# Performance work log

Measured on AMD Instinct MI355X. Metric: run time of the kernel, lower is better.

## Reference

```python
import jax, jax.numpy as jnp
import numpy as np
from jax import lax

B, S, H, T = 64, 512, 1024, 48


def setup_inputs() -> dict:
    key = jax.random.key(0)
    ks = jax.random.split(key, 8)
    x = jax.random.normal(ks[0], (B, S, H), dtype=jnp.float32)
    # left-aligned variable-length attention mask (lengths in [S//2, S])
    lengths = jax.random.randint(ks[1], (B,), S // 2, S + 1)
    attention_mask = (jnp.arange(S)[None, :] < lengths[:, None]).astype(jnp.int32)
    labels = jax.random.randint(ks[2], (B, S), 0, T).astype(jnp.int64)
    # decoder Linear(H, T)
    W = jax.random.normal(ks[3], (H, T), dtype=jnp.float32) / np.sqrt(H)
    b = jnp.zeros((T,), dtype=jnp.float32)
    # CRF parameters (allennlp-style: transitions + start/end transitions)
    transitions = jax.random.normal(ks[4], (T, T), dtype=jnp.float32) * 0.1
    start_trans = jax.random.normal(ks[5], (T,), dtype=jnp.float32) * 0.1
    end_trans = jax.random.normal(ks[6], (T,), dtype=jnp.float32) * 0.1
    return {"x": x, "attention_mask": attention_mask, "labels": labels,
            "W": W, "b": b, "transitions": transitions,
            "start_trans": start_trans, "end_trans": end_trans}


def _log_partition(logits, mask, trans, start, end):
    # logits [B,S,T], mask [B,S] int. Returns logZ [B].
    alpha0 = start[None, :] + logits[:, 0]                     # [B,T]
    emits = jnp.moveaxis(logits[:, 1:], 1, 0)                  # [S-1,B,T]
    ms = mask[:, 1:].T                                         # [S-1,B]

    def step(alpha, inp):
        emit, m = inp
        inner = alpha[:, :, None] + trans[None, :, :] + emit[:, None, :]  # [B,T,T]
        new = jax.nn.logsumexp(inner, axis=1)
        alpha = jnp.where(m[:, None] > 0, new, alpha)
        return alpha, None

    alpha, _ = lax.scan(step, alpha0, (emits, ms))
    return jax.nn.logsumexp(alpha + end[None, :], axis=1)      # [B]


def _gold_score(logits, labels, mask, trans, start, end):
    maskf = mask.astype(logits.dtype)
    emit = jnp.take_along_axis(logits, labels[..., None], axis=2)[..., 0]  # [B,S]
    emit_score = jnp.sum(emit * maskf, axis=1)
    tr = trans[labels[:, :-1], labels[:, 1:]]                   # [B,S-1]
    trans_score = jnp.sum(tr * maskf[:, 1:], axis=1)
    last_idx = jnp.sum(mask, axis=1) - 1                        # [B]
    last_tags = jnp.take_along_axis(labels, last_idx[:, None], axis=1)[:, 0]
    return start[labels[:, 0]] + emit_score + trans_score + end[last_tags]


def _viterbi(logits, mask, trans, start, end):
    Bn, Sn, Tn = logits.shape
    v0 = start[None, :] + logits[:, 0]
    emits = jnp.moveaxis(logits[:, 1:], 1, 0)                  # [S-1,B,T]
    ms = mask[:, 1:].T
    ident = jnp.broadcast_to(jnp.arange(Tn, dtype=jnp.int32)[None, :], (Bn, Tn))

    def step(v, inp):
        emit, m = inp
        scores = v[:, :, None] + trans[None, :, :]              # [B,T_prev,T_cur]
        bp = jnp.argmax(scores, axis=1).astype(jnp.int32)       # [B,T]
        best = jnp.max(scores, axis=1) + emit
        v_new = jnp.where(m[:, None] > 0, best, v)
        bp = jnp.where(m[:, None] > 0, bp, ident)               # identity at padded steps
        return v_new, bp

    v, bps = lax.scan(step, v0, (emits, ms))                    # bps [S-1,B,T]
    last = jnp.argmax(v + end[None, :], axis=1).astype(jnp.int32)  # [B]

    def back(tag, bp):
        prev = jnp.take_along_axis(bp, tag[:, None], axis=1)[:, 0]
        return prev, tag

    first_tag, rest = lax.scan(back, last, bps, reverse=True)   # rest [S-1,B]
    tags = jnp.concatenate([first_tag[:, None], rest.T], axis=1)  # [B,S]
    return (tags * mask).astype(jnp.int64)                      # pad with zeros


def reference(x, attention_mask, labels, W, b, transitions, start_trans, end_trans):
    features = jnp.einsum('bsh,ht->bst', x, W) + b              # decoder Linear
    pred_labels = _viterbi(features, attention_mask, transitions, start_trans, end_trans)
    logZ = _log_partition(features, attention_mask, transitions, start_trans, end_trans)
    gold = _gold_score(features, labels, attention_mask, transitions, start_trans, end_trans)
    loss = -jnp.sum(gold - logZ)                                # -log-likelihood, summed over batch
    return features, pred_labels, loss
```

## Files before the change

### kernel.cpp

```cpp
#include <hip/hip_runtime.h>
#include <hip/hip_bf16.h>
#include <math.h>

#define Bn 64
#define Sn 512
#define Hn 1024
#define Tn 48

#define LOG2E 1.4426950408889634f
#define LN2f  0.6931471805599453f

#define PRED_OFF (Bn*Sn*Tn)
#define LOSS_OFF (PRED_OFF + Bn*Sn)

#define RL(x,i) __int_as_float(__builtin_amdgcn_readlane(__float_as_int(x),(i)))

#if __has_builtin(__builtin_amdgcn_exp2f)
#define EXP2(x) __builtin_amdgcn_exp2f(x)
#else
#define EXP2(x) exp2f(x)
#endif
#if __has_builtin(__builtin_amdgcn_logf)
#define LOG2(x) __builtin_amdgcn_logf(x)
#else
#define LOG2(x) log2f(x)
#endif

__device__ __forceinline__ unsigned umin2(unsigned a, unsigned b) { return a < b ? a : b; }

#define DOT4(ACC,A,B) { ACC = fmaf((A).x,(B).x,ACC); ACC = fmaf((A).y,(B).y,ACC); ACC = fmaf((A).z,(B).z,ACC); ACC = fmaf((A).w,(B).w,ACC); }

__global__ __launch_bounds__(256) void gemm_feat(
    const float* __restrict__ x, const float* __restrict__ W,
    const float* __restrict__ bias, float* __restrict__ feat)
{
  __shared__ __align__(16) float xs[64][68];
  __shared__ __align__(16) float wsT[Tn][68];
  const int tid = threadIdx.x;
  const int srow = tid >> 2;
  const int sqc  = tid & 3;
  const int ty = tid >> 3;
  const int tx = tid & 7;
  const size_t row0 = (size_t)blockIdx.x * 64;

  float4 xreg[4];
  float  wreg[12];
  #pragma unroll
  for (int p = 0; p < 4; ++p)
    xreg[p] = *reinterpret_cast<const float4*>(&x[(row0 + srow)*Hn + (sqc + p*4)*4]);
  #pragma unroll
  for (int i = 0; i < 12; ++i) {
    const int id = tid + i*256; const int kk = id/Tn; const int t = id - kk*Tn;
    wreg[i] = W[(size_t)kk*Tn + t];
  }

  float acc[2][6];
  #pragma unroll
  for (int r = 0; r < 2; ++r)
    #pragma unroll
    for (int c = 0; c < 6; ++c) acc[r][c] = 0.f;

  for (int k0 = 0; k0 < Hn; k0 += 64) {
    #pragma unroll
    for (int p = 0; p < 4; ++p)
      *reinterpret_cast<float4*>(&xs[srow][(sqc + p*4)*4]) = xreg[p];
    #pragma unroll
    for (int i = 0; i < 12; ++i) {
      const int id = tid + i*256; const int kk = id/Tn; const int t = id - kk*Tn;
      wsT[t][kk] = wreg[i];
    }
    __syncthreads();
    if (k0 + 64 < Hn) {
      #pragma unroll
      for (int p = 0; p < 4; ++p)
        xreg[p] = *reinterpret_cast<const float4*>(&x[(row0 + srow)*Hn + (k0+64) + (sqc + p*4)*4]);
      #pragma unroll
      for (int i = 0; i < 12; ++i) {
        const int id = tid + i*256; const int kk = id/Tn; const int t = id - kk*Tn;
        wreg[i] = W[(size_t)(k0 + 64 + kk)*Tn + t];
      }
    }
    #pragma unroll 4
    for (int kk = 0; kk < 64; kk += 4) {
      const float4 a0 = *reinterpret_cast<const float4*>(&xs[ty*2+0][kk]);
      const float4 a1 = *reinterpret_cast<const float4*>(&xs[ty*2+1][kk]);
      const float4 w0 = *reinterpret_cast<const float4*>(&wsT[tx*6+0][kk]);
      const float4 w1 = *reinterpret_cast<const float4*>(&wsT[tx*6+1][kk]);
      const float4 w2 = *reinterpret_cast<const float4*>(&wsT[tx*6+2][kk]);
      const float4 w3 = *reinterpret_cast<const float4*>(&wsT[tx*6+3][kk]);
      const float4 w4 = *reinterpret_cast<const float4*>(&wsT[tx*6+4][kk]);
      const float4 w5 = *reinterpret_cast<const float4*>(&wsT[tx*6+5][kk]);
      DOT4(acc[0][0],a0,w0) DOT4(acc[0][1],a0,w1) DOT4(acc[0][2],a0,w2)
      DOT4(acc[0][3],a0,w3) DOT4(acc[0][4],a0,w4) DOT4(acc[0][5],a0,w5)
      DOT4(acc[1][0],a1,w0) DOT4(acc[1][1],a1,w1) DOT4(acc[1][2],a1,w2)
      DOT4(acc[1][3],a1,w3) DOT4(acc[1][4],a1,w4) DOT4(acc[1][5],a1,w5)
    }
    __syncthreads();
  }
  #pragma unroll
  for (int c = 0; c < 6; ++c) {
    const int col = tx*6 + c;
    const float bv = bias[col];
    #pragma unroll
    for (int r = 0; r < 2; ++r)
      feat[(row0 + ty*2 + r)*Tn + col] = acc[r][c] + bv;
  }
}

__global__ __launch_bounds__(64, 1) void crf_kernel(
    const float* __restrict__ feat,
    const int* __restrict__ mask,
    const int* __restrict__ labels,
    const float* __restrict__ trans,
    const float* __restrict__ startv,
    const float* __restrict__ endv,
    float* __restrict__ pred_out,
    float* __restrict__ wsLogZ,
    float* __restrict__ wsGold)
{
  __shared__ unsigned char bpL[Sn * 64];
  __shared__ unsigned char pathL[384 * 64];
  __shared__ __align__(16) float slds[64];
  __shared__ int EA[8];

  const int role = blockIdx.x >> 6;
  const int b    = blockIdx.x & 63;
  const int lane = threadIdx.x;
  const float* fb = feat + (size_t)b * Sn * Tn;

  int lc = 0;
  #pragma unroll
  for (int it = 0; it < Sn/64; ++it) lc += (mask[(size_t)b*Sn + it*64 + lane] != 0);
  #pragma unroll
  for (int off = 32; off; off >>= 1) lc += __shfl_xor(lc, off);
  const int len = lc;

  const int j = (lane < Tn) ? lane : (Tn - 1);
  const float4* sv4 = reinterpret_cast<const float4*>(slds);

  if (role == 0) {
    float Ev[48];
    #pragma unroll
    for (int i = 0; i < 48; ++i) Ev[i] = EXP2(trans[i*Tn + j] * LOG2E);
    const float a0 = (startv[j] + fb[j]) * LOG2E;
    float Zref = RL(a0, 0);
    float beta = a0 - Zref;
    slds[lane] = EXP2(beta);
    float em2 = fb[Tn + j] * LOG2E;
    for (int t = 1; t < len; ++t) {
      const int tn = (t + 1 < len) ? (t + 1) : t;
      const float em_nxt = fb[(size_t)tn*Tn + j] * LOG2E;
      float4 av[12];
      #pragma unroll
      for (int k = 0; k < 12; ++k) av[k] = sv4[k];
      float s0=0.f, s1=0.f, s2=0.f, s3=0.f;
      #pragma unroll
      for (int k = 0; k < 12; ++k) {
        s0 = fmaf(av[k].x, Ev[4*k+0], s0);
        s1 = fmaf(av[k].y, Ev[4*k+1], s1);
        s2 = fmaf(av[k].z, Ev[4*k+2], s2);
        s3 = fmaf(av[k].w, Ev[4*k+3], s3);
      }
      const float dj = LOG2((s0 + s1) + (s2 + s3)) + em2;
      const float d0 = RL(dj, 0);
      Zref += d0;
      const float nb = dj - d0;
      slds[lane] = EXP2(nb);
      beta = nb;
      em2 = em_nxt;
    }
    float fv = (lane < Tn) ? beta + endv[lane] * LOG2E : -INFINITY;
    float m = fv;
    #pragma unroll
    for (int off = 32; off; off >>= 1) m = fmaxf(m, __shfl_xor(m, off));
    float e = (lane < Tn) ? EXP2(fv - m) : 0.f;
    #pragma unroll
    for (int off = 32; off; off >>= 1) e += __shfl_xor(e, off);
    if (lane == 0) wsLogZ[b] = (Zref + m + LOG2(e)) * LN2f;

  } else if (role == 1) {
    float trv[48];
    #pragma unroll
    for (int i = 0; i < 48; ++i) trv[i] = trans[i*Tn + j];
    float v = startv[j] + fb[j];
    slds[lane] = v;
    float em_cur = fb[Tn + j];
    for (int t = 1; t < len; ++t) {
      const int tn = (t + 1 < len) ? (t + 1) : t;
      const float em_nxt = fb[(size_t)tn*Tn + j];
      float4 av[12];
      #pragma unroll
      for (int k = 0; k < 12; ++k) av[k] = sv4[k];
      float q[48];
      #pragma unroll
      for (int k = 0; k < 12; ++k) {
        q[4*k+0] = av[k].x + trv[4*k+0];
        q[4*k+1] = av[k].y + trv[4*k+1];
        q[4*k+2] = av[k].z + trv[4*k+2];
        q[4*k+3] = av[k].w + trv[4*k+3];
      }
      float m16[16];
      #pragma unroll
      for (int u = 0; u < 16; ++u)
        m16[u] = fmaxf(fmaxf(q[3*u], q[3*u+1]), q[3*u+2]);
      float m6a = fmaxf(fmaxf(m16[0],  m16[1]),  m16[2]);
      float m6b = fmaxf(fmaxf(m16[3],  m16[4]),  m16[5]);
      float m6c = fmaxf(fmaxf(m16[6],  m16[7]),  m16[8]);
      float m6d = fmaxf(fmaxf(m16[9],  m16[10]), m16[11]);
      float m6e = fmaxf(fmaxf(m16[12], m16[13]), m16[14]);
      float m6f = m16[15];
      const float best = fmaxf(fmaxf(fmaxf(m6a,m6b),m6c),
                               fmaxf(fmaxf(m6d,m6e),m6f));
      unsigned s16[16];
      #pragma unroll
      for (int u = 0; u < 16; ++u) {
        const unsigned ka = __float_as_uint(q[3*u]   - best) | (unsigned)(3*u);
        const unsigned kb = __float_as_uint(q[3*u+1] - best) | (unsigned)(3*u+1);
        const unsigned kc = __float_as_uint(q[3*u+2] - best) | (unsigned)(3*u+2);
        s16[u] = umin2(umin2(ka, kb), kc);
      }
      unsigned i6a = umin2(umin2(s16[0],  s16[1]),  s16[2]);
      unsigned i6b = umin2(umin2(s16[3],  s16[4]),  s16[5]);
      unsigned i6c = umin2(umin2(s16[6],  s16[7]),  s16[8]);
      unsigned i6d = umin2(umin2(s16[9],  s16[10]), s16[11]);
      unsigned i6e = umin2(umin2(s16[12], s16[13]), s16[14]);
      unsigned i6f = s16[15];
      const unsigned bidx = umin2(umin2(umin2(i6a,i6b),i6c), umin2(umin2(i6d,i6e),i6f));
      bpL[t*64 + lane] = (unsigned char)bidx;
      v = best + em_cur;
      slds[lane] = v;
      em_cur = em_nxt;
    }
    for (int t = len; t < Sn; ++t) bpL[t*64 + lane] = (unsigned char)lane;

    float fv = (lane < Tn) ? v + endv[lane] : -INFINITY;
    int fi = (lane < Tn) ? lane : 64;
    #pragma unroll
    for (int off = 32; off; off >>= 1) {
      const float ov = __shfl_xor(fv, off);
      const int   oi = __shfl_xor(fi, off);
      if (ov > fv || (ov == fv && oi < fi)) { fv = ov; fi = oi; }
    }
    __syncthreads();

    #define JOB(r) \
      const int id##r  = lane + 64*(r); \
      const int seg##r = id##r & 7;     \
      int cur##r = id##r >> 3;          \
      const int bpb##r = seg##r << 12;  \
      const int pb##r  = id##r << 6;    \
      pathL[pb##r + 63] = (unsigned char)cur##r;
    JOB(0) JOB(1) JOB(2) JOB(3) JOB(4) JOB(5)
    for (int d = 62; d >= 0; --d) {
      const int o = (d + 1) << 6;
      cur0 = bpL[bpb0 + o + cur0]; pathL[pb0 + d] = (unsigned char)cur0;
      cur1 = bpL[bpb1 + o + cur1]; pathL[pb1 + d] = (unsigned char)cur1;
      cur2 = bpL[bpb2 + o + cur2]; pathL[pb2 + d] = (unsigned char)cur2;
      cur3 = bpL[bpb3 + o + cur3]; pathL[pb3 + d] = (unsigned char)cur3;
      cur4 = bpL[bpb4 + o + cur4]; pathL[pb4 + d] = (unsigned char)cur4;
      cur5 = bpL[bpb5 + o + cur5]; pathL[pb5 + d] = (unsigned char)cur5;
    }
    #undef JOB
    __syncthreads();
    if (lane == 0) {
      int Ecur = fi;
      EA[7] = Ecur;
      for (int s = 7; s >= 1; --s) {
        const int bottom = pathL[((Ecur << 3) + s) * 64];
        Ecur = bpL[(s << 12) + bottom];
        EA[s-1] = Ecur;
      }
    }
    __syncthreads();
    #pragma unroll
    for (int r8 = 0; r8 < 8; ++r8) {
      const int t = r8*64 + lane;
      const int pv = pathL[((EA[r8] << 3) + r8) * 64 + lane];
      pred_out[(size_t)b*Sn + t] = (t < len) ? (float)pv : 0.f;
    }

  } else {
    float g = 0.f;
    #pragma unroll
    for (int it = 0; it < Sn/64; ++it) {
      const int sg = it*64 + lane;
      if (sg < len) {
        const int la = labels[(size_t)b*Sn + sg];
        float e = fb[(size_t)sg*Tn + la];
        if (sg > 0) e += trans[labels[(size_t)b*Sn + sg - 1]*Tn + la];
        g += e;
      }
    }
    #pragma unroll
    for (int off = 32; off; off >>= 1) g += __shfl_xor(g, off);
    if (lane == 0) {
      g += startv[labels[(size_t)b*Sn]] + endv[labels[(size_t)b*Sn + len - 1]];
      wsGold[b] = g;
    }
  }
}

__global__ void loss_reduce(const float* __restrict__ wsLogZ,
                            const float* __restrict__ wsGold,
                            float* __restrict__ out)
{
  const int lane = threadIdx.x;
  float v = wsLogZ[lane] - wsGold[lane];
  #pragma unroll
  for (int off = 32; off; off >>= 1) v += __shfl_xor(v, off);
  if (lane == 0) out[0] = v;
}

extern "C" void kernel_launch(void* const* d_in, const int* in_sizes, int n_in,
                              void* d_out, int out_size, void* d_ws, size_t ws_size,
                              hipStream_t stream) {
  const float* x      = (const float*)d_in[0];
  const int*   mask   = (const int*)  d_in[1];
  const int*   labels = (const int*)  d_in[2];
  const float* W      = (const float*)d_in[3];
  const float* bias   = (const float*)d_in[4];
  const float* trans  = (const float*)d_in[5];
  const float* startv = (const float*)d_in[6];
  const float* endv   = (const float*)d_in[7];

  float* out  = (float*)d_out;
  float* feat = out;
  float* pred = out + PRED_OFF;
  float* loss = out + LOSS_OFF;
  float* wsLogZ = (float*)d_ws;
  float* wsGold = wsLogZ + 64;

  gemm_feat<<<(Bn*Sn)/64, 256, 0, stream>>>(x, W, bias, feat);
  crf_kernel<<<192, 64, 0, stream>>>(feat, mask, labels, trans, startv, endv, pred, wsLogZ, wsGold);
  loss_reduce<<<1, 64, 0, stream>>>(wsLogZ, wsGold, loss);
}
```

Before: 323.9 us.

## Restructure feature GEMM tiling and prefetch CRF emissions eight steps ahead

The GEMM now gives each block 128 rows. Each wave computes 12 output columns for two rows per lane, reading W directly from global memory with wave-uniform addresses instead of staging it in shared memory. The forward and Viterbi recurrences in the CRF kernel keep an 8-deep register queue of emission loads, so global load latency is hidden several steps ahead. The Viterbi step also writes the new score before doing the argmax backpointer work, which shortens the serial dependency chain. The trade-offs are half as many GEMM blocks and the per-iteration W loads now going through the scalar or global cache path.

```diff
diff --git a/kernel.cpp b/kernel.cpp
--- a/kernel.cpp
+++ b/kernel.cpp
@@ -28,82 +28,65 @@
 
 __device__ __forceinline__ unsigned umin2(unsigned a, unsigned b) { return a < b ? a : b; }
 
-#define DOT4(ACC,A,B) { ACC = fmaf((A).x,(B).x,ACC); ACC = fmaf((A).y,(B).y,ACC); ACC = fmaf((A).z,(B).z,ACC); ACC = fmaf((A).w,(B).w,ACC); }
-
 __global__ __launch_bounds__(256) void gemm_feat(
     const float* __restrict__ x, const float* __restrict__ W,
     const float* __restrict__ bias, float* __restrict__ feat)
 {
-  __shared__ __align__(16) float xs[64][68];
-  __shared__ __align__(16) float wsT[Tn][68];
-  const int tid = threadIdx.x;
-  const int srow = tid >> 2;
-  const int sqc  = tid & 3;
-  const int ty = tid >> 3;
-  const int tx = tid & 7;
-  const size_t row0 = (size_t)blockIdx.x * 64;
-
-  float4 xreg[4];
-  float  wreg[12];
-  #pragma unroll
-  for (int p = 0; p < 4; ++p)
-    xreg[p] = *reinterpret_cast<const float4*>(&x[(row0 + srow)*Hn + (sqc + p*4)*4]);
-  #pragma unroll
-  for (int i = 0; i < 12; ++i) {
-    const int id = tid + i*256; const int kk = id/Tn; const int t = id - kk*Tn;
-    wreg[i] = W[(size_t)kk*Tn + t];
-  }
-
-  float acc[2][6];
-  #pragma unroll
-  for (int r = 0; r < 2; ++r)
-    #pragma unroll
-    for (int c = 0; c < 6; ++c) acc[r][c] = 0.f;
+  __shared__ float xs[128][65];
+  const int tid  = threadIdx.x;
+  const int lane = tid & 63;
+  const int col0 = __builtin_amdgcn_readfirstlane((tid >> 6) * 12);
+  const size_t row0 = (size_t)blockIdx.x * 128;
+
+  const int srow = tid >> 1;
+  const int skk0 = (tid & 1) * 32;
+
+  const int r0 = lane;
+  const int r1 = lane + 64;
+
+  float4 xreg[8];
+  #pragma unroll
+  for (int p = 0; p < 8; ++p)
+    xreg[p] = *reinterpret_cast<const float4*>(&x[(row0 + srow)*Hn + skk0 + p*4]);
+
+  float acc0[12], acc1[12];
+  #pragma unroll
+  for (int c = 0; c < 12; ++c) { acc0[c] = 0.f; acc1[c] = 0.f; }
 
   for (int k0 = 0; k0 < Hn; k0 += 64) {
     #pragma unroll
-    for (int p = 0; p < 4; ++p)
-      *reinterpret_cast<float4*>(&xs[srow][(sqc + p*4)*4]) = xreg[p];
-    #pragma unroll
-    for (int i = 0; i < 12; ++i) {
-      const int id = tid + i*256; const int kk = id/Tn; const int t = id - kk*Tn;
-      wsT[t][kk] = wreg[i];
+    for (int p = 0; p < 8; ++p) {
+      xs[srow][skk0 + p*4 + 0] = xreg[p].x;
+      xs[srow][skk0 + p*4 + 1] = xreg[p].y;
+      xs[srow][skk0 + p*4 + 2] = xreg[p].z;
+      xs[srow][skk0 + p*4 + 3] = xreg[p].w;
     }
     __syncthreads();
     if (k0 + 64 < Hn) {
       #pragma unroll
-      for (int p = 0; p < 4; ++p)
-        xreg[p] = *reinterpret_cast<const float4*>(&x[(row0 + srow)*Hn + (k0+64) + (sqc + p*4)*4]);
+      for (int p = 0; p < 8; ++p)
+        xreg[p] = *reinterpret_cast<const float4*>(&x[(row0 + srow)*Hn + (k0+64) + skk0 + p*4]);
+    }
+    const float* Wk = W + (size_t)k0 * Tn + col0;
+    #pragma unroll 4
+    for (int kk = 0; kk < 64; ++kk) {
+      const float a0 = xs[r0][kk];
+      const float a1 = xs[r1][kk];
+      const float* wrow = Wk + kk * Tn;
       #pragma unroll
-      for (int i = 0; i < 12; ++i) {
-        const int id = tid + i*256; const int kk = id/Tn; const int t = id - kk*Tn;
-        wreg[i] = W[(size_t)(k0 + 64 + kk)*Tn + t];
-      }
-    }
-    #pragma unroll 4
-    for (int kk = 0; kk < 64; kk += 4) {
-      const float4 a0 = *reinterpret_cast<const float4*>(&xs[ty*2+0][kk]);
-      const float4 a1 = *reinterpret_cast<const float4*>(&xs[ty*2+1][kk]);
-      const float4 w0 = *reinterpret_cast<const float4*>(&wsT[tx*6+0][kk]);
-      const float4 w1 = *reinterpret_cast<const float4*>(&wsT[tx*6+1][kk]);
-      const float4 w2 = *reinterpret_cast<const float4*>(&wsT[tx*6+2][kk]);
-      const float4 w3 = *reinterpret_cast<const float4*>(&wsT[tx*6+3][kk]);
-      const float4 w4 = *reinterpret_cast<const float4*>(&wsT[tx*6+4][kk]);
-      const float4 w5 = *reinterpret_cast<const float4*>(&wsT[tx*6+5][kk]);
-      DOT4(acc[0][0],a0,w0) DOT4(acc[0][1],a0,w1) DOT4(acc[0][2],a0,w2)
-      DOT4(acc[0][3],a0,w3) DOT4(acc[0][4],a0,w4) DOT4(acc[0][5],a0,w5)
-      DOT4(acc[1][0],a1,w0) DOT4(acc[1][1],a1,w1) DOT4(acc[1][2],a1,w2)
-      DOT4(acc[1][3],a1,w3) DOT4(acc[1][4],a1,w4) DOT4(acc[1][5],a1,w5)
+      for (int c = 0; c < 12; ++c) {
+        const float wv_ = wrow[c];
+        acc0[c] = fmaf(a0, wv_, acc0[c]);
+        acc1[c] = fmaf(a1, wv_, acc1[c]);
+      }
     }
     __syncthreads();
   }
   #pragma unroll
-  for (int c = 0; c < 6; ++c) {
-    const int col = tx*6 + c;
-    const float bv = bias[col];
-    #pragma unroll
-    for (int r = 0; r < 2; ++r)
-      feat[(row0 + ty*2 + r)*Tn + col] = acc[r][c] + bv;
+  for (int c = 0; c < 12; ++c) {
+    const float bv = bias[col0 + c];
+    feat[(row0 + r0)*Tn + col0 + c] = acc0[c] + bv;
+    feat[(row0 + r1)*Tn + col0 + c] = acc1[c] + bv;
   }
 }
 
@@ -142,32 +125,43 @@
     float Ev[48];
     #pragma unroll
     for (int i = 0; i < 48; ++i) Ev[i] = EXP2(trans[i*Tn + j] * LOG2E);
+    float emq[8];
+    #pragma unroll
+    for (int d = 0; d < 8; ++d) {
+      int s = 1 + d; s = s < len ? s : len - 1;
+      emq[d] = fb[(size_t)s * Tn + j];
+    }
     const float a0 = (startv[j] + fb[j]) * LOG2E;
     float Zref = RL(a0, 0);
     float beta = a0 - Zref;
     slds[lane] = EXP2(beta);
-    float em2 = fb[Tn + j] * LOG2E;
-    for (int t = 1; t < len; ++t) {
-      const int tn = (t + 1 < len) ? (t + 1) : t;
-      const float em_nxt = fb[(size_t)tn*Tn + j] * LOG2E;
-      float4 av[12];
+    for (int t = 1; t < len; t += 8) {
       #pragma unroll
-      for (int k = 0; k < 12; ++k) av[k] = sv4[k];
-      float s0=0.f, s1=0.f, s2=0.f, s3=0.f;
-      #pragma unroll
-      for (int k = 0; k < 12; ++k) {
-        s0 = fmaf(av[k].x, Ev[4*k+0], s0);
-        s1 = fmaf(av[k].y, Ev[4*k+1], s1);
-        s2 = fmaf(av[k].z, Ev[4*k+2], s2);
-        s3 = fmaf(av[k].w, Ev[4*k+3], s3);
-      }
-      const float dj = LOG2((s0 + s1) + (s2 + s3)) + em2;
-      const float d0 = RL(dj, 0);
-      Zref += d0;
-      const float nb = dj - d0;
-      slds[lane] = EXP2(nb);
-      beta = nb;
-      em2 = em_nxt;
+      for (int u = 0; u < 8; ++u) {
+        const int tt = t + u;
+        if (tt < len) {
+          const float em2 = emq[u] * LOG2E;
+          int tf = tt + 8; tf = tf < len ? tf : len - 1;
+          emq[u] = fb[(size_t)tf * Tn + j];
+          float4 av[12];
+          #pragma unroll
+          for (int k = 0; k < 12; ++k) av[k] = sv4[k];
+          float s0=0.f, s1=0.f, s2=0.f, s3=0.f;
+          #pragma unroll
+          for (int k = 0; k < 12; ++k) {
+            s0 = fmaf(av[k].x, Ev[4*k+0], s0);
+            s1 = fmaf(av[k].y, Ev[4*k+1], s1);
+            s2 = fmaf(av[k].z, Ev[4*k+2], s2);
+            s3 = fmaf(av[k].w, Ev[4*k+3], s3);
+          }
+          const float dj = LOG2((s0 + s1) + (s2 + s3)) + em2;
+          const float d0 = RL(dj, 0);
+          const float nb = dj - d0;
+          slds[lane] = EXP2(nb);
+          Zref += d0;
+          beta = nb;
+        }
+      }
     }
     float fv = (lane < Tn) ? beta + endv[lane] * LOG2E : -INFINITY;
     float m = fv;
@@ -182,54 +176,65 @@
     float trv[48];
     #pragma unroll
     for (int i = 0; i < 48; ++i) trv[i] = trans[i*Tn + j];
+    float emq[8];
+    #pragma unroll
+    for (int d = 0; d < 8; ++d) {
+      int s = 1 + d; s = s < len ? s : len - 1;
+      emq[d] = fb[(size_t)s * Tn + j];
+    }
     float v = startv[j] + fb[j];
     slds[lane] = v;
-    float em_cur = fb[Tn + j];
-    for (int t = 1; t < len; ++t) {
-      const int tn = (t + 1 < len) ? (t + 1) : t;
-      const float em_nxt = fb[(size_t)tn*Tn + j];
-      float4 av[12];
+    for (int t = 1; t < len; t += 8) {
       #pragma unroll
-      for (int k = 0; k < 12; ++k) av[k] = sv4[k];
-      float q[48];
-      #pragma unroll
-      for (int k = 0; k < 12; ++k) {
-        q[4*k+0] = av[k].x + trv[4*k+0];
-        q[4*k+1] = av[k].y + trv[4*k+1];
-        q[4*k+2] = av[k].z + trv[4*k+2];
-        q[4*k+3] = av[k].w + trv[4*k+3];
-      }
-      float m16[16];
-      #pragma unroll
-      for (int u = 0; u < 16; ++u)
-        m16[u] = fmaxf(fmaxf(q[3*u], q[3*u+1]), q[3*u+2]);
-      float m6a = fmaxf(fmaxf(m16[0],  m16[1]),  m16[2]);
-      float m6b = fmaxf(fmaxf(m16[3],  m16[4]),  m16[5]);
-      float m6c = fmaxf(fmaxf(m16[6],  m16[7]),  m16[8]);
-      float m6d = fmaxf(fmaxf(m16[9],  m16[10]), m16[11]);
-      float m6e = fmaxf(fmaxf(m16[12], m16[13]), m16[14]);
-      float m6f = m16[15];
-      const float best = fmaxf(fmaxf(fmaxf(m6a,m6b),m6c),
-                               fmaxf(fmaxf(m6d,m6e),m6f));
-      unsigned s16[16];
-      #pragma unroll
-      for (int u = 0; u < 16; ++u) {
-        const unsigned ka = __float_as_uint(q[3*u]   - best) | (unsigned)(3*u);
-        const unsigned kb = __float_as_uint(q[3*u+1] - best) | (unsigned)(3*u+1);
-        const unsigned kc = __float_as_uint(q[3*u+2] - best) | (unsigned)(3*u+2);
-        s16[u] = umin2(umin2(ka, kb), kc);
-      }
-      unsigned i6a = umin2(umin2(s16[0],  s16[1]),  s16[2]);
-      unsigned i6b = umin2(umin2(s16[3],  s16[4]),  s16[5]);
-      unsigned i6c = umin2(umin2(s16[6],  s16[7]),  s16[8]);
-      unsigned i6d = umin2(umin2(s16[9],  s16[10]), s16[11]);
-      unsigned i6e = umin2(umin2(s16[12], s16[13]), s16[14]);
-      unsigned i6f = s16[15];
-      const unsigned bidx = umin2(umin2(umin2(i6a,i6b),i6c), umin2(umin2(i6d,i6e),i6f));
-      bpL[t*64 + lane] = (unsigned char)bidx;
-      v = best + em_cur;
-      slds[lane] = v;
-      em_cur = em_nxt;
+      for (int u = 0; u < 8; ++u) {
+        const int tt = t + u;
+        if (tt < len) {
+          const float em_cur = emq[u];
+          int tf = tt + 8; tf = tf < len ? tf : len - 1;
+          emq[u] = fb[(size_t)tf * Tn + j];
+          float4 av[12];
+          #pragma unroll
+          for (int k = 0; k < 12; ++k) av[k] = sv4[k];
+          float q[48];
+          #pragma unroll
+          for (int k = 0; k < 12; ++k) {
+            q[4*k+0] = av[k].x + trv[4*k+0];
+            q[4*k+1] = av[k].y + trv[4*k+1];
+            q[4*k+2] = av[k].z + trv[4*k+2];
+            q[4*k+3] = av[k].w + trv[4*k+3];
+          }
+          float m16[16];
+          #pragma unroll
+          for (int uu = 0; uu < 16; ++uu)
+            m16[uu] = fmaxf(fmaxf(q[3*uu], q[3*uu+1]), q[3*uu+2]);
+          float m6a = fmaxf(fmaxf(m16[0],  m16[1]),  m16[2]);
+          float m6b = fmaxf(fmaxf(m16[3],  m16[4]),  m16[5]);
+          float m6c = fmaxf(fmaxf(m16[6],  m16[7]),  m16[8]);
+          float m6d = fmaxf(fmaxf(m16[9],  m16[10]), m16[11]);
+          float m6e = fmaxf(fmaxf(m16[12], m16[13]), m16[14]);
+          float m6f = m16[15];
+          const float best = fmaxf(fmaxf(fmaxf(m6a,m6b),m6c),
+                                   fmaxf(fmaxf(m6d,m6e),m6f));
+          v = best + em_cur;
+          slds[lane] = v;
+          unsigned s16[16];
+          #pragma unroll
+          for (int uu = 0; uu < 16; ++uu) {
+            const unsigned ka = __float_as_uint(q[3*uu]   - best) | (unsigned)(3*uu);
+            const unsigned kb = __float_as_uint(q[3*uu+1] - best) | (unsigned)(3*uu+1);
+            const unsigned kc = __float_as_uint(q[3*uu+2] - best) | (unsigned)(3*uu+2);
+            s16[uu] = umin2(umin2(ka, kb), kc);
+          }
+          unsigned i6a = umin2(umin2(s16[0],  s16[1]),  s16[2]);
+          unsigned i6b = umin2(umin2(s16[3],  s16[4]),  s16[5]);
+          unsigned i6c = umin2(umin2(s16[6],  s16[7]),  s16[8]);
+          unsigned i6d = umin2(umin2(s16[9],  s16[10]), s16[11]);
+          unsigned i6e = umin2(umin2(s16[12], s16[13]), s16[14]);
+          unsigned i6f = s16[15];
+          const unsigned bidx = umin2(umin2(umin2(i6a,i6b),i6c), umin2(umin2(i6d,i6e),i6f));
+          bpL[tt*64 + lane] = (unsigned char)bidx;
+        }
+      }
     }
     for (int t = len; t < Sn; ++t) bpL[t*64 + lane] = (unsigned char)lane;
 
@@ -330,7 +335,7 @@
   float* wsLogZ = (float*)d_ws;
   float* wsGold = wsLogZ + 64;
 
-  gemm_feat<<<(Bn*Sn)/64, 256, 0, stream>>>(x, W, bias, feat);
+  gemm_feat<<<(Bn*Sn)/128, 256, 0, stream>>>(x, W, bias, feat);
   crf_kernel<<<192, 64, 0, stream>>>(feat, mask, labels, trans, startv, endv, pred, wsLogZ, wsGold);
   loss_reduce<<<1, 64, 0, stream>>>(wsLogZ, wsGold, loss);
 }
```

Measured after the change: 334.3 us. +3.2%, slower.
